# Performance work log

Measured on AMD Instinct MI355X. Metric: run time of the kernel, lower is better.

The kernel has to match this reference:

```python
import jax, jax.numpy as jnp
import numpy as np

FG_THR = 0.7
BG_THR = 0.3
NUM_PER_IMAGE = 256
NUM_POS_MAX = int(NUM_PER_IMAGE * 0.5)  # positive_ratio = 0.5
BBOX_W = (1.0, 1.0, 1.0, 1.0)
BETA = 1.0 / 9.0


def _permute(t, C):
    # N x (A*C) x H x W -> N x (H*W*A) x C, matching RPNLoss.permute
    N, _, H, W = t.shape
    t = t.reshape(N, -1, C, H, W)
    t = jnp.transpose(t, (0, 3, 4, 1, 2))
    return t.reshape(N, -1, C)


def _iou(a, b):
    # a: [N,4], b: [M,4] -> [N,M] (with +1 box convention, as in source)
    x_tl = jnp.maximum(a[:, None, 0], b[None, :, 0])
    y_tl = jnp.maximum(a[:, None, 1], b[None, :, 1])
    x_rb = jnp.minimum(a[:, None, 2], b[None, :, 2])
    y_rb = jnp.minimum(a[:, None, 3], b[None, :, 3])
    inter = jnp.clip(x_rb - x_tl + 1.0, 0.0) * jnp.clip(y_rb - y_tl + 1.0, 0.0)
    area1 = (a[:, 2] - a[:, 0] + 1.0) * (a[:, 3] - a[:, 1] + 1.0)
    area2 = (b[:, 2] - b[:, 0] + 1.0) * (b[:, 3] - b[:, 1] + 1.0)
    return inter / (area1[:, None] + area2[None, :] - inter)


def _encode(anchors, targets):
    ws = anchors[:, 2] - anchors[:, 0] + 1.0
    hs = anchors[:, 3] - anchors[:, 1] + 1.0
    x_ctr = anchors[:, 0] + 0.5 * ws
    y_ctr = anchors[:, 1] + 0.5 * hs
    t_ws = targets[:, 2] - targets[:, 0] + 1.0
    t_hs = targets[:, 3] - targets[:, 1] + 1.0
    t_x = targets[:, 0] + 0.5 * t_ws
    t_y = targets[:, 1] + 0.5 * t_hs
    wx, wy, ww, wh = BBOX_W
    tx = wx * (t_x - x_ctr) / ws
    ty = wy * (t_y - y_ctr) / hs
    tw = ww * jnp.log(t_ws / ws)
    th = wh * jnp.log(t_hs / hs)
    return jnp.stack([tx, ty, tw, th], axis=1)


def _bce_logits(l, t):
    return jnp.maximum(l, 0.0) - l * t + jnp.log1p(jnp.exp(-jnp.abs(l)))


def _per_image(anchor, logit, breg, size, target, key):
    N = anchor.shape[0]
    ious = _iou(anchor, target)  # [N, M]
    vals = ious.max(axis=1)
    ori = jnp.argmax(ious, axis=1).astype(jnp.int32)
    inds = jnp.where(vals < BG_THR, -1, ori)
    inds = jnp.where((vals >= BG_THR) & (vals < FG_THR), -2, inds)
    # low-quality matches: anchors achieving the per-target max IoU keep their argmax
    col_max = ious.max(axis=0)
    restore = (ious == col_max[None, :]).any(axis=1)
    inds = jnp.where(restore, ori, inds)
    # filter_anchors: keep anchors fully inside the image (size = (h, w))
    inside = (anchor[:, 0] >= 0) & (anchor[:, 1] >= 0) & \
             (anchor[:, 2] <= size[1] - 1.0) & (anchor[:, 3] <= size[0] - 1.0)
    inds = jnp.where(inside, inds, -2)

    pos = inds >= 0
    neg = inds == -1
    # random sampling via random priorities + fixed-size top_k with validity masks
    r = jax.random.uniform(key, (N,))
    pos_vals, pos_idx = jax.lax.top_k(jnp.where(pos, r, -1.0), NUM_POS_MAX)
    valid_pos = pos_vals >= 0.0
    num_pos = valid_pos.sum()
    neg_vals, neg_idx = jax.lax.top_k(jnp.where(neg, r, -1.0), NUM_PER_IMAGE)
    valid_neg = (neg_vals >= 0.0) & (jnp.arange(NUM_PER_IMAGE) < (NUM_PER_IMAGE - num_pos))

    # classification loss terms (BCE with logits); pos target 1, neg target 0
    vp = valid_pos.astype(logit.dtype)
    vn = valid_neg.astype(logit.dtype)
    cls_sum = jnp.sum(_bce_logits(logit[pos_idx], 1.0) * vp) + \
              jnp.sum(_bce_logits(logit[neg_idx], 0.0) * vn)
    count = num_pos + valid_neg.sum()

    m = jnp.clip(inds[pos_idx], 0, None)
    offsets = _encode(anchor[pos_idx], target[m])
    diff = jnp.abs(breg[pos_idx] - offsets)
    sl1 = jnp.where(diff < BETA, 0.5 * diff * diff / BETA, diff - 0.5 * BETA)
    reg_sum = jnp.sum(sl1 * vp[:, None])
    return cls_sum, count, reg_sum


def reference(anchors, logits, bbox_regs, sizes, targets):
    B = anchors.shape[0]
    log = _permute(logits, 1)[..., 0]      # [B, H*W*A]
    breg = _permute(bbox_regs, 4)          # [B, H*W*A, 4]
    keys = jax.random.split(jax.random.key(42), B)
    cls_s, cnt, reg_s = jax.vmap(_per_image)(anchors, log, breg, sizes, targets, keys)
    total = jnp.sum(cnt).astype(anchors.dtype)
    cls_loss = jnp.sum(cls_s) / total
    reg_loss = jnp.sum(reg_s) / total
    return jnp.stack([cls_loss, reg_loss])


def setup_inputs() -> dict:
    key = jax.random.key(0)
    ks = jax.random.split(key, 10)
    B, A, H, W, M = 4, 3, 168, 256, 32
    N = H * W * A
    IMG_H, IMG_W = 800.0, 1333.0
    x1 = jax.random.uniform(ks[0], (B, N)) * 1200.0
    y1 = jax.random.uniform(ks[1], (B, N)) * 700.0
    aw = jax.random.uniform(ks[2], (B, N)) * 300.0 + 16.0
    ah = jax.random.uniform(ks[3], (B, N)) * 300.0 + 16.0
    anchors = jnp.stack([x1, y1, x1 + aw, y1 + ah], axis=-1)  # some out of image -> filtered
    tx1 = jax.random.uniform(ks[4], (B, M)) * 1000.0
    ty1 = jax.random.uniform(ks[5], (B, M)) * 500.0
    tw = jax.random.uniform(ks[6], (B, M)) * 250.0 + 30.0
    th = jax.random.uniform(ks[7], (B, M)) * 200.0 + 30.0
    targets = jnp.stack([tx1, ty1, jnp.minimum(tx1 + tw, IMG_W - 1.0),
                         jnp.minimum(ty1 + th, IMG_H - 1.0)], axis=-1)
    logits = jax.random.normal(ks[8], (B, A, H, W), dtype=jnp.float32)
    bbox_regs = jax.random.normal(ks[9], (B, 4 * A, H, W), dtype=jnp.float32) * 0.1
    sizes = jnp.tile(jnp.array([IMG_H, IMG_W], dtype=jnp.float32), (B, 1))
    return {"anchors": anchors, "logits": logits, "bbox_regs": bbox_regs,
            "sizes": sizes, "targets": targets}
```

## Files before the change

kernel.cpp:

```cpp
#include <hip/hip_runtime.h>
#include <stdint.h>

#define Bn 4
#define An 3
#define Hn 168
#define Wn 256
#define Mn 32
#define HWn (Hn*Wn)
#define Nn (HWn*An)
#define POS_CAP 8192
#define BND_CAP 2048
#define NPERIM 256
#define NPOSMAX 128
#define FG_THR 0.7f
#define BG_THR 0.3f
#define BETA (1.0f/9.0f)

#define NBLK 126
#define APT 4
#define STRIDE (NBLK * 256)
#define SEG 1024

#define OFF_POSCNT 0
#define OFF_BNDCNT 4
#define OFF_BOUND  8
#define OFF_NEED   12
#define OFF_COUNT  16
#define OFF_CLS    17
#define OFF_REG    18
#define OFF_DONE   19
#define OFF_KEYS   24
#define OFF_PCM    32
#define OFF_NSEGC  16160
#define OFF_PHIST  16664
#define OFF_PLIST  532760
#define OFF_BLIST  598296
#define OFF_NLIST  614680

__device__ __forceinline__ uint32_t rotl32(uint32_t v, int n) { return (v << n) | (v >> (32 - n)); }

__device__ __forceinline__ void tf2x32(uint32_t k0, uint32_t k1, uint32_t x0, uint32_t x1,
                                       uint32_t& o0, uint32_t& o1) {
    uint32_t k2 = k0 ^ k1 ^ 0x1BD11BDAu;
    x0 += k0; x1 += k1;
    x0 += x1; x1 = rotl32(x1, 13); x1 ^= x0;
    x0 += x1; x1 = rotl32(x1, 15); x1 ^= x0;
    x0 += x1; x1 = rotl32(x1, 26); x1 ^= x0;
    x0 += x1; x1 = rotl32(x1, 6);  x1 ^= x0;
    x0 += k1; x1 += k2 + 1u;
    x0 += x1; x1 = rotl32(x1, 17); x1 ^= x0;
    x0 += x1; x1 = rotl32(x1, 29); x1 ^= x0;
    x0 += x1; x1 = rotl32(x1, 16); x1 ^= x0;
    x0 += x1; x1 = rotl32(x1, 24); x1 ^= x0;
    x0 += k2; x1 += k0 + 2u;
    x0 += x1; x1 = rotl32(x1, 13); x1 ^= x0;
    x0 += x1; x1 = rotl32(x1, 15); x1 ^= x0;
    x0 += x1; x1 = rotl32(x1, 26); x1 ^= x0;
    x0 += x1; x1 = rotl32(x1, 6);  x1 ^= x0;
    x0 += k0; x1 += k1 + 3u;
    x0 += x1; x1 = rotl32(x1, 17); x1 ^= x0;
    x0 += x1; x1 = rotl32(x1, 29); x1 ^= x0;
    x0 += x1; x1 = rotl32(x1, 16); x1 ^= x0;
    x0 += x1; x1 = rotl32(x1, 24); x1 ^= x0;
    x0 += k1; x1 += k2 + 4u;
    x0 += x1; x1 = rotl32(x1, 13); x1 ^= x0;
    x0 += x1; x1 = rotl32(x1, 15); x1 ^= x0;
    x0 += x1; x1 = rotl32(x1, 26); x1 ^= x0;
    x0 += x1; x1 = rotl32(x1, 6);  x1 ^= x0;
    x0 += k2; x1 += k0 + 5u;
    o0 = x0; o1 = x1;
}

__device__ __forceinline__ uint32_t rng_m23(uint32_t k0, uint32_t k1, uint32_t i) {
    uint32_t o0, o1;
    tf2x32(k0, k1, 0u, i, o0, o1);
    return (o0 ^ o1) >> 9;
}

__device__ __forceinline__ float iou_one(float a0, float a1, float a2, float a3,
                                         float t0, float t1, float t2, float t3) {
    float xtl = fmaxf(a0, t0), ytl = fmaxf(a1, t1);
    float xrb = fminf(a2, t2), yrb = fminf(a3, t3);
    float iw = fmaxf(xrb - xtl + 1.0f, 0.0f);
    float ih = fmaxf(yrb - ytl + 1.0f, 0.0f);
    float inter = iw * ih;
    float area1 = (a2 - a0 + 1.0f) * (a3 - a1 + 1.0f);
    float area2 = (t2 - t0 + 1.0f) * (t3 - t1 + 1.0f);
    return inter * __builtin_amdgcn_rcpf(area1 + area2 - inter);
}

__global__ void __launch_bounds__(256) k1_colmax(const float* __restrict__ anchors,
                                                 const float* __restrict__ targets,
                                                 uint32_t* __restrict__ ws) {
    int b = blockIdx.y, j = blockIdx.x, tid = threadIdx.x;
    if (b == 0 && j == 0) {
        if (tid < 24) ws[tid] = 0u;
        if (tid == 0) {
            for (int bb = 0; bb < Bn; ++bb) {
                uint32_t o0, o1;
                tf2x32(0u, 42u, 0u, (uint32_t)bb, o0, o1);
                ws[OFF_KEYS + 2*bb] = o0; ws[OFF_KEYS + 2*bb + 1] = o1;
            }
        }
    }
    __shared__ float part[4][Mn];
    int base = j * 256 + tid;
    float4 a[APT];
    #pragma unroll
    for (int k = 0; k < APT; ++k)
        a[k] = ((const float4*)anchors)[b * Nn + base + k * STRIDE];
    float cm[Mn];
    #pragma unroll 4
    for (int t = 0; t < Mn; ++t) {
        float4 tv = ((const float4*)targets)[b * Mn + t];
        float m0 = 0.0f;
        #pragma unroll
        for (int k = 0; k < APT; ++k)
            m0 = fmaxf(m0, iou_one(a[k].x, a[k].y, a[k].z, a[k].w, tv.x, tv.y, tv.z, tv.w));
        cm[t] = m0;
    }
    #pragma unroll
    for (int t = 0; t < Mn; ++t) {
        #pragma unroll
        for (int o = 32; o > 0; o >>= 1) cm[t] = fmaxf(cm[t], __shfl_xor(cm[t], o, 64));
    }
    int wid = tid >> 6, lane = tid & 63;
    if (lane == 0) {
        #pragma unroll
        for (int t = 0; t < Mn; ++t) part[wid][t] = cm[t];
    }
    __syncthreads();
    if (tid < Mn) {
        float v = fmaxf(fmaxf(part[0][tid], part[1][tid]),
                        fmaxf(part[2][tid], part[3][tid]));
        ws[OFF_PCM + ((size_t)b * NBLK + j) * Mn + tid] = __float_as_uint(v);
    }
}

__global__ void __launch_bounds__(256) k2_cat(const float* __restrict__ anchors,
                                              const float* __restrict__ targets,
                                              const float* __restrict__ sizes,
                                              uint32_t* __restrict__ ws) {
    int b = blockIdx.y, j = blockIdx.x, tid = threadIdx.x;
    __shared__ float cmf[Mn];
    __shared__ float redf[256];
    __shared__ uint32_t lh[1024];
    __shared__ uint32_t segcnt;
    {
        int t = tid & 31, sub = tid >> 5;
        float acc = 0.0f;
        for (int jj = sub; jj < NBLK; jj += 8)
            acc = fmaxf(acc, __uint_as_float(ws[OFF_PCM + ((size_t)b * NBLK + jj) * Mn + t]));
        redf[tid] = acc;
        __syncthreads();
        if (sub == 0) {
            #pragma unroll
            for (int q = 1; q < 8; ++q) acc = fmaxf(acc, redf[t + 32 * q]);
            cmf[t] = acc;
        }
    }
    #pragma unroll
    for (int q = 0; q < 4; ++q) lh[tid + 256 * q] = 0u;
    if (tid == 0) segcnt = 0u;
    __syncthreads();

    int base = j * 256 + tid;
    float4 av[APT];
    #pragma unroll
    for (int k = 0; k < APT; ++k)
        av[k] = ((const float4*)anchors)[b * Nn + base + k * STRIDE];
    float rowmax[APT]; int ori[APT]; bool restore[APT];
    #pragma unroll
    for (int k = 0; k < APT; ++k) { rowmax[k] = -1.0f; ori[k] = 0; restore[k] = false; }
    #pragma unroll 4
    for (int t = 0; t < Mn; ++t) {
        float4 tv = ((const float4*)targets)[b * Mn + t];
        float cmv = cmf[t];
        #pragma unroll
        for (int k = 0; k < APT; ++k) {
            float iou = iou_one(av[k].x, av[k].y, av[k].z, av[k].w, tv.x, tv.y, tv.z, tv.w);
            if (iou > rowmax[k]) { rowmax[k] = iou; ori[k] = t; }
            restore[k] = restore[k] || (iou == cmv);
        }
    }
    float sh = sizes[b * 2 + 0], sw = sizes[b * 2 + 1];
    uint32_t key0 = ws[OFF_KEYS + 2 * b], key1 = ws[OFF_KEYS + 2 * b + 1];
    int lane = tid & 63;
    unsigned long long lt_mask = (lane == 63) ? 0x7FFFFFFFFFFFFFFFull : ((1ull << lane) - 1ull);
    uint2* nseg = (uint2*)(ws + OFF_NLIST) + (size_t)(b * NBLK + j) * SEG;
    #pragma unroll
    for (int k = 0; k < APT; ++k) {
        int i = base + k * STRIDE;
        bool inside = (av[k].x >= 0.0f) && (av[k].y >= 0.0f) &&
                      (av[k].z <= sw - 1.0f) && (av[k].w <= sh - 1.0f);
        uint32_t cat = 0;
        if (inside) {
            if (restore[k] || rowmax[k] >= FG_THR) cat = 2;
            else if (rowmax[k] < BG_THR) cat = 1;
        }
        uint32_t m = rng_m23(key0, key1, (uint32_t)i);
        unsigned long long pmask = __ballot(cat == 2u);
        if (pmask) {
            int leader = __ffsll((long long)pmask) - 1;
            uint32_t bb = 0;
            if (lane == leader) bb = atomicAdd(&ws[OFF_POSCNT + b], (uint32_t)__popcll(pmask));
            bb = __shfl(bb, leader, 64);
            if (cat == 2u) {
                uint32_t p = bb + (uint32_t)__popcll(pmask & lt_mask);
                if (p < POS_CAP)
                    ((uint2*)(ws + OFF_PLIST))[(size_t)b * POS_CAP + p] =
                        make_uint2(m, (uint32_t)i | ((uint32_t)ori[k] << 17));
            }
        }
        unsigned long long nmask = __ballot(cat == 1u);
        if (nmask) {
            int leader = __ffsll((long long)nmask) - 1;
            uint32_t bb = 0;
            if (lane == leader) bb = atomicAdd(&segcnt, (uint32_t)__popcll(nmask));
            bb = __shfl(bb, leader, 64);
            if (cat == 1u) {
                uint32_t p = bb + (uint32_t)__popcll(nmask & lt_mask);
                nseg[p] = make_uint2(m, (uint32_t)i);
                atomicAdd(&lh[m >> 13], 1u);
            }
        }
    }
    __syncthreads();
    uint32_t* slice = ws + OFF_PHIST + ((size_t)b * NBLK + j) * 1024;
    #pragma unroll
    for (int q = 0; q < 4; ++q) slice[tid + 256 * q] = lh[tid + 256 * q];
    if (tid == 0) ws[OFF_NSEGC + b * NBLK + j] = segcnt;
}

__global__ void __launch_bounds__(256) k25_bound(uint32_t* __restrict__ ws) {
    int b = blockIdx.x, t = threadIdx.x;
    __shared__ uint32_t csum[256];
    uint4 h = make_uint4(0, 0, 0, 0);
    const uint32_t* ph = ws + OFF_PHIST + (size_t)b * NBLK * 1024;
    for (int s = 0; s < NBLK; ++s) {
        uint4 v = ((const uint4*)(ph + (size_t)s * 1024))[t];
        h.x += v.x; h.y += v.y; h.z += v.z; h.w += v.w;
    }
    uint32_t sum = h.x + h.y + h.z + h.w;
    csum[t] = sum;
    __syncthreads();
    for (int off = 1; off < 256; off <<= 1) {
        uint32_t mine = csum[t];
        uint32_t add = (t + off < 256) ? csum[t + off] : 0u;
        __syncthreads();
        csum[t] = mine + add;
        __syncthreads();
    }
    uint32_t pc = ws[OFF_POSCNT + b];
    int num_pos = (pc < (uint32_t)NPOSMAX) ? (int)pc : NPOSMAX;
    int k_neg = NPERIM - num_pos;
    uint32_t total = csum[0];
    if ((int)total < k_neg) {
        if (t == 0) {
            ws[OFF_BOUND + b] = 0xFFFFFFFFu;
            ws[OFF_NEED + b] = 0u;
            atomicAdd(&ws[OFF_COUNT], (uint32_t)(num_pos + (int)total));
        }
        return;
    }
    uint32_t incl = csum[t];
    uint32_t next = (t < 255) ? csum[t + 1] : 0u;
    if ((int)incl >= k_neg && (int)next < k_neg) {
        int cum = (int)next;
        uint32_t hv[4] = { h.x, h.y, h.z, h.w };
        int boundary = -1, needed = 0;
        #pragma unroll
        for (int q = 3; q >= 0; --q) {
            int c = (int)hv[q];
            if (cum + c >= k_neg) { boundary = 4 * t + q; needed = k_neg - cum; break; }
            cum += c;
        }
        ws[OFF_BOUND + b] = (uint32_t)boundary;
        ws[OFF_NEED + b] = (uint32_t)needed;
        atomicAdd(&ws[OFF_COUNT], (uint32_t)(num_pos + k_neg));
    }
}

__global__ void __launch_bounds__(256) k3_neg(const float* __restrict__ logits,
                                              uint32_t* __restrict__ ws) {
    int b = blockIdx.y, j = blockIdx.x;
    int bd = (int)(int32_t)ws[OFF_BOUND + b];
    int cnt = (int)ws[OFF_NSEGC + b * NBLK + j];
    const uint2* nseg = (const uint2*)(ws + OFF_NLIST) + (size_t)(b * NBLK + j) * SEG;
    float local = 0.0f;
    for (int idx = (int)threadIdx.x; idx < cnt; idx += 256) {
        uint2 e = nseg[idx];
        int bk = (int)(e.x >> 13);
        if (bk > bd) {
            int i = (int)e.y;
            int a = i % An, hw = i / An;
            float l = logits[(b * An + a) * HWn + hw];
            local += fmaxf(l, 0.0f) + log1pf(expf(-fabsf(l)));
        } else if (bk == bd) {
            uint32_t q = atomicAdd(&ws[OFF_BNDCNT + b], 1u);
            if (q < BND_CAP)
                ((uint2*)(ws + OFF_BLIST))[(size_t)b * BND_CAP + q] = e;
        }
    }
    __shared__ float red[256];
    red[threadIdx.x] = local;
    __syncthreads();
    for (int s = 128; s > 0; s >>= 1) {
        if ((int)threadIdx.x < s) red[threadIdx.x] += red[threadIdx.x + s];
        __syncthreads();
    }
    if (threadIdx.x == 0 && red[0] != 0.0f) atomicAdd((float*)&ws[OFF_CLS], red[0]);
}

__device__ __forceinline__ bool sel_less(uint2 a, uint2 b) {
    return (a.x > b.x) || (a.x == b.x && a.y < b.y);
}

__device__ void bitonic_sort_shared(uint2* buf, int n) {
    for (int k = 2; k <= n; k <<= 1) {
        for (int j = k >> 1; j > 0; j >>= 1) {
            for (int t = (int)threadIdx.x; t < n; t += 256) {
                int ixj = t ^ j;
                if (ixj > t) {
                    uint2 x = buf[t], y = buf[ixj];
                    bool up = ((t & k) == 0);
                    bool sw = up ? sel_less(y, x) : sel_less(x, y);
                    if (sw) { buf[t] = y; buf[ixj] = x; }
                }
            }
            __syncthreads();
        }
    }
}

__global__ void __launch_bounds__(256) k4_final(const float* __restrict__ anchors,
                                                const float* __restrict__ targets,
                                                const float* __restrict__ logits,
                                                const float* __restrict__ bregs,
                                                uint32_t* __restrict__ ws,
                                                float* __restrict__ out) {
    int b = blockIdx.x, tid = threadIdx.x;
    __shared__ uint2 buf[BND_CAP];
    __shared__ float red[256];
    float cls = 0.0f, reg = 0.0f;

    uint32_t pcu = ws[OFF_POSCNT + b];
    int pc = (pcu < (uint32_t)POS_CAP) ? (int)pcu : POS_CAP;
    const uint2* plist = (const uint2*)(ws + OFF_PLIST) + (size_t)b * POS_CAP;
    int psel = (pc < NPOSMAX) ? pc : NPOSMAX;
    bool use_buf = false;
    if (pc > NPOSMAX) {
        int n = (pc < BND_CAP) ? pc : BND_CAP;
        for (int t = tid; t < n; t += 256) buf[t] = plist[t];
        int npad = 1; while (npad < n) npad <<= 1;
        for (int t = tid; t < npad; t += 256) if (t >= n) buf[t] = make_uint2(0u, 0xFFFFFFFFu);
        __syncthreads();
        bitonic_sort_shared(buf, npad);
        use_buf = true;
        psel = (NPOSMAX < n) ? NPOSMAX : n;
    }
    for (int t = tid; t < psel; t += 256) {
        uint32_t packed = use_buf ? buf[t].y : plist[t].y;
        int i = (int)(packed & 0x1FFFFu);
        int ori = (int)(packed >> 17);
        int a = i % An, hw = i / An;
        float l = logits[(b * An + a) * HWn + hw];
        cls += fmaxf(l, 0.0f) - l + log1pf(expf(-fabsf(l)));
        float4 av = ((const float4*)anchors)[b * Nn + i];
        float4 tv = ((const float4*)targets)[b * Mn + ori];
        float aws = av.z - av.x + 1.0f, ahs = av.w - av.y + 1.0f;
        float axc = av.x + 0.5f * aws, ayc = av.y + 0.5f * ahs;
        float tws = tv.z - tv.x + 1.0f, ths = tv.w - tv.y + 1.0f;
        float txc = tv.x + 0.5f * tws, tyc = tv.y + 0.5f * ths;
        float off0 = (txc - axc) / aws;
        float off1 = (tyc - ayc) / ahs;
        float off2 = logf(tws / aws);
        float off3 = logf(ths / ahs);
        float br0 = bregs[(b * 12 + a * 4 + 0) * HWn + hw];
        float br1 = bregs[(b * 12 + a * 4 + 1) * HWn + hw];
        float br2 = bregs[(b * 12 + a * 4 + 2) * HWn + hw];
        float br3 = bregs[(b * 12 + a * 4 + 3) * HWn + hw];
        float d;
        d = fabsf(br0 - off0); reg += (d < BETA) ? 0.5f * d * d / BETA : d - 0.5f * BETA;
        d = fabsf(br1 - off1); reg += (d < BETA) ? 0.5f * d * d / BETA : d - 0.5f * BETA;
        d = fabsf(br2 - off2); reg += (d < BETA) ? 0.5f * d * d / BETA : d - 0.5f * BETA;
        d = fabsf(br3 - off3); reg += (d < BETA) ? 0.5f * d * d / BETA : d - 0.5f * BETA;
    }
    __syncthreads();

    int need = (int)ws[OFF_NEED + b];
    if (need > 0) {
        uint32_t nbu = ws[OFF_BNDCNT + b];
        int nb = (nbu < (uint32_t)BND_CAP) ? (int)nbu : BND_CAP;
        const uint2* blist = (const uint2*)(ws + OFF_BLIST) + (size_t)b * BND_CAP;
        for (int t = tid; t < nb; t += 256) buf[t] = blist[t];
        int npad = 1; while (npad < nb) npad <<= 1;
        for (int t = tid; t < npad; t += 256) if (t >= nb) buf[t] = make_uint2(0u, 0xFFFFFFFFu);
        __syncthreads();
        bitonic_sort_shared(buf, npad);
        int sel = (need < nb) ? need : nb;
        for (int t = tid; t < sel; t += 256) {
            int i = (int)buf[t].y;
            int a = i % An, hw = i / An;
            float l = logits[(b * An + a) * HWn + hw];
            cls += fmaxf(l, 0.0f) + log1pf(expf(-fabsf(l)));
        }
    }

    red[tid] = cls;
    __syncthreads();
    for (int s = 128; s > 0; s >>= 1) {
        if (tid < s) red[tid] += red[tid + s];
        __syncthreads();
    }
    if (tid == 0 && red[0] != 0.0f) atomicAdd((float*)&ws[OFF_CLS], red[0]);
    __syncthreads();
    red[tid] = reg;
    __syncthreads();
    for (int s = 128; s > 0; s >>= 1) {
        if (tid < s) red[tid] += red[tid + s];
        __syncthreads();
    }
    if (tid == 0) {
        if (red[0] != 0.0f) atomicAdd((float*)&ws[OFF_REG], red[0]);
        __threadfence();
        uint32_t old = atomicAdd(&ws[OFF_DONE], 1u);
        if (old == Bn - 1) {
            float cls_tot = __uint_as_float(atomicAdd(&ws[OFF_CLS], 0u));
            float reg_tot = __uint_as_float(atomicAdd(&ws[OFF_REG], 0u));
            float cnt = (float)atomicAdd(&ws[OFF_COUNT], 0u);
            out[0] = cls_tot / cnt;
            out[1] = reg_tot / cnt;
        }
    }
}

extern "C" void kernel_launch(void* const* d_in, const int* in_sizes, int n_in,
                              void* d_out, int out_size, void* d_ws, size_t ws_size,
                              hipStream_t stream) {
    const float* anchors = (const float*)d_in[0];
    const float* logits  = (const float*)d_in[1];
    const float* bregs   = (const float*)d_in[2];
    const float* sizes   = (const float*)d_in[3];
    const float* targets = (const float*)d_in[4];
    float* out = (float*)d_out;
    uint32_t* ws = (uint32_t*)d_ws;

    k1_colmax<<<dim3(NBLK, Bn), dim3(256), 0, stream>>>(anchors, targets, ws);
    k2_cat<<<dim3(NBLK, Bn), dim3(256), 0, stream>>>(anchors, targets, sizes, ws);
    k25_bound<<<dim3(Bn), dim3(256), 0, stream>>>(ws);
    k3_neg<<<dim3(NBLK, Bn), dim3(256), 0, stream>>>(logits, ws);
    k4_final<<<dim3(Bn), dim3(256), 0, stream>>>(anchors, targets, logits, bregs, ws, out);
}
```

Baseline: 158.1 us.

## Fuse all RPN loss stages into one cooperative kernel with grid syncs

```diff
diff --git a/kernel.cpp b/kernel.cpp
--- a/kernel.cpp
+++ b/kernel.cpp
@@ -1,5 +1,8 @@
 #include <hip/hip_runtime.h>
+#include <hip/hip_cooperative_groups.h>
 #include <stdint.h>
+
+namespace cg = cooperative_groups;
 
 #define Bn 4
 #define An 3
@@ -32,10 +35,11 @@
 #define OFF_KEYS   24
 #define OFF_PCM    32
 #define OFF_NSEGC  16160
-#define OFF_PHIST  16664
-#define OFF_PLIST  532760
-#define OFF_BLIST  598296
-#define OFF_NLIST  614680
+#define OFF_PLIST  16664
+#define OFF_BLIST  82200
+#define OFF_NLIST  98584
+#define OFF_WPCM   1130776
+#define OFF_GHIST  1195288
 
 __device__ __forceinline__ uint32_t rotl32(uint32_t v, int n) { return (v << n) | (v >> (32 - n)); }
 
@@ -89,229 +93,6 @@
     return inter * __builtin_amdgcn_rcpf(area1 + area2 - inter);
 }
 
-__global__ void __launch_bounds__(256) k1_colmax(const float* __restrict__ anchors,
-                                                 const float* __restrict__ targets,
-                                                 uint32_t* __restrict__ ws) {
-    int b = blockIdx.y, j = blockIdx.x, tid = threadIdx.x;
-    if (b == 0 && j == 0) {
-        if (tid < 24) ws[tid] = 0u;
-        if (tid == 0) {
-            for (int bb = 0; bb < Bn; ++bb) {
-                uint32_t o0, o1;
-                tf2x32(0u, 42u, 0u, (uint32_t)bb, o0, o1);
-                ws[OFF_KEYS + 2*bb] = o0; ws[OFF_KEYS + 2*bb + 1] = o1;
-            }
-        }
-    }
-    __shared__ float part[4][Mn];
-    int base = j * 256 + tid;
-    float4 a[APT];
-    #pragma unroll
-    for (int k = 0; k < APT; ++k)
-        a[k] = ((const float4*)anchors)[b * Nn + base + k * STRIDE];
-    float cm[Mn];
-    #pragma unroll 4
-    for (int t = 0; t < Mn; ++t) {
-        float4 tv = ((const float4*)targets)[b * Mn + t];
-        float m0 = 0.0f;
-        #pragma unroll
-        for (int k = 0; k < APT; ++k)
-            m0 = fmaxf(m0, iou_one(a[k].x, a[k].y, a[k].z, a[k].w, tv.x, tv.y, tv.z, tv.w));
-        cm[t] = m0;
-    }
-    #pragma unroll
-    for (int t = 0; t < Mn; ++t) {
-        #pragma unroll
-        for (int o = 32; o > 0; o >>= 1) cm[t] = fmaxf(cm[t], __shfl_xor(cm[t], o, 64));
-    }
-    int wid = tid >> 6, lane = tid & 63;
-    if (lane == 0) {
-        #pragma unroll
-        for (int t = 0; t < Mn; ++t) part[wid][t] = cm[t];
-    }
-    __syncthreads();
-    if (tid < Mn) {
-        float v = fmaxf(fmaxf(part[0][tid], part[1][tid]),
-                        fmaxf(part[2][tid], part[3][tid]));
-        ws[OFF_PCM + ((size_t)b * NBLK + j) * Mn + tid] = __float_as_uint(v);
-    }
-}
-
-__global__ void __launch_bounds__(256) k2_cat(const float* __restrict__ anchors,
-                                              const float* __restrict__ targets,
-                                              const float* __restrict__ sizes,
-                                              uint32_t* __restrict__ ws) {
-    int b = blockIdx.y, j = blockIdx.x, tid = threadIdx.x;
-    __shared__ float cmf[Mn];
-    __shared__ float redf[256];
-    __shared__ uint32_t lh[1024];
-    __shared__ uint32_t segcnt;
-    {
-        int t = tid & 31, sub = tid >> 5;
-        float acc = 0.0f;
-        for (int jj = sub; jj < NBLK; jj += 8)
-            acc = fmaxf(acc, __uint_as_float(ws[OFF_PCM + ((size_t)b * NBLK + jj) * Mn + t]));
-        redf[tid] = acc;
-        __syncthreads();
-        if (sub == 0) {
-            #pragma unroll
-            for (int q = 1; q < 8; ++q) acc = fmaxf(acc, redf[t + 32 * q]);
-            cmf[t] = acc;
-        }
-    }
-    #pragma unroll
-    for (int q = 0; q < 4; ++q) lh[tid + 256 * q] = 0u;
-    if (tid == 0) segcnt = 0u;
-    __syncthreads();
-
-    int base = j * 256 + tid;
-    float4 av[APT];
-    #pragma unroll
-    for (int k = 0; k < APT; ++k)
-        av[k] = ((const float4*)anchors)[b * Nn + base + k * STRIDE];
-    float rowmax[APT]; int ori[APT]; bool restore[APT];
-    #pragma unroll
-    for (int k = 0; k < APT; ++k) { rowmax[k] = -1.0f; ori[k] = 0; restore[k] = false; }
-    #pragma unroll 4
-    for (int t = 0; t < Mn; ++t) {
-        float4 tv = ((const float4*)targets)[b * Mn + t];
-        float cmv = cmf[t];
-        #pragma unroll
-        for (int k = 0; k < APT; ++k) {
-            float iou = iou_one(av[k].x, av[k].y, av[k].z, av[k].w, tv.x, tv.y, tv.z, tv.w);
-            if (iou > rowmax[k]) { rowmax[k] = iou; ori[k] = t; }
-            restore[k] = restore[k] || (iou == cmv);
-        }
-    }
-    float sh = sizes[b * 2 + 0], sw = sizes[b * 2 + 1];
-    uint32_t key0 = ws[OFF_KEYS + 2 * b], key1 = ws[OFF_KEYS + 2 * b + 1];
-    int lane = tid & 63;
-    unsigned long long lt_mask = (lane == 63) ? 0x7FFFFFFFFFFFFFFFull : ((1ull << lane) - 1ull);
-    uint2* nseg = (uint2*)(ws + OFF_NLIST) + (size_t)(b * NBLK + j) * SEG;
-    #pragma unroll
-    for (int k = 0; k < APT; ++k) {
-        int i = base + k * STRIDE;
-        bool inside = (av[k].x >= 0.0f) && (av[k].y >= 0.0f) &&
-                      (av[k].z <= sw - 1.0f) && (av[k].w <= sh - 1.0f);
-        uint32_t cat = 0;
-        if (inside) {
-            if (restore[k] || rowmax[k] >= FG_THR) cat = 2;
-            else if (rowmax[k] < BG_THR) cat = 1;
-        }
-        uint32_t m = rng_m23(key0, key1, (uint32_t)i);
-        unsigned long long pmask = __ballot(cat == 2u);
-        if (pmask) {
-            int leader = __ffsll((long long)pmask) - 1;
-            uint32_t bb = 0;
-            if (lane == leader) bb = atomicAdd(&ws[OFF_POSCNT + b], (uint32_t)__popcll(pmask));
-            bb = __shfl(bb, leader, 64);
-            if (cat == 2u) {
-                uint32_t p = bb + (uint32_t)__popcll(pmask & lt_mask);
-                if (p < POS_CAP)
-                    ((uint2*)(ws + OFF_PLIST))[(size_t)b * POS_CAP + p] =
-                        make_uint2(m, (uint32_t)i | ((uint32_t)ori[k] << 17));
-            }
-        }
-        unsigned long long nmask = __ballot(cat == 1u);
-        if (nmask) {
-            int leader = __ffsll((long long)nmask) - 1;
-            uint32_t bb = 0;
-            if (lane == leader) bb = atomicAdd(&segcnt, (uint32_t)__popcll(nmask));
-            bb = __shfl(bb, leader, 64);
-            if (cat == 1u) {
-                uint32_t p = bb + (uint32_t)__popcll(nmask & lt_mask);
-                nseg[p] = make_uint2(m, (uint32_t)i);
-                atomicAdd(&lh[m >> 13], 1u);
-            }
-        }
-    }
-    __syncthreads();
-    uint32_t* slice = ws + OFF_PHIST + ((size_t)b * NBLK + j) * 1024;
-    #pragma unroll
-    for (int q = 0; q < 4; ++q) slice[tid + 256 * q] = lh[tid + 256 * q];
-    if (tid == 0) ws[OFF_NSEGC + b * NBLK + j] = segcnt;
-}
-
-__global__ void __launch_bounds__(256) k25_bound(uint32_t* __restrict__ ws) {
-    int b = blockIdx.x, t = threadIdx.x;
-    __shared__ uint32_t csum[256];
-    uint4 h = make_uint4(0, 0, 0, 0);
-    const uint32_t* ph = ws + OFF_PHIST + (size_t)b * NBLK * 1024;
-    for (int s = 0; s < NBLK; ++s) {
-        uint4 v = ((const uint4*)(ph + (size_t)s * 1024))[t];
-        h.x += v.x; h.y += v.y; h.z += v.z; h.w += v.w;
-    }
-    uint32_t sum = h.x + h.y + h.z + h.w;
-    csum[t] = sum;
-    __syncthreads();
-    for (int off = 1; off < 256; off <<= 1) {
-        uint32_t mine = csum[t];
-        uint32_t add = (t + off < 256) ? csum[t + off] : 0u;
-        __syncthreads();
-        csum[t] = mine + add;
-        __syncthreads();
-    }
-    uint32_t pc = ws[OFF_POSCNT + b];
-    int num_pos = (pc < (uint32_t)NPOSMAX) ? (int)pc : NPOSMAX;
-    int k_neg = NPERIM - num_pos;
-    uint32_t total = csum[0];
-    if ((int)total < k_neg) {
-        if (t == 0) {
-            ws[OFF_BOUND + b] = 0xFFFFFFFFu;
-            ws[OFF_NEED + b] = 0u;
-            atomicAdd(&ws[OFF_COUNT], (uint32_t)(num_pos + (int)total));
-        }
-        return;
-    }
-    uint32_t incl = csum[t];
-    uint32_t next = (t < 255) ? csum[t + 1] : 0u;
-    if ((int)incl >= k_neg && (int)next < k_neg) {
-        int cum = (int)next;
-        uint32_t hv[4] = { h.x, h.y, h.z, h.w };
-        int boundary = -1, needed = 0;
-        #pragma unroll
-        for (int q = 3; q >= 0; --q) {
-            int c = (int)hv[q];
-            if (cum + c >= k_neg) { boundary = 4 * t + q; needed = k_neg - cum; break; }
-            cum += c;
-        }
-        ws[OFF_BOUND + b] = (uint32_t)boundary;
-        ws[OFF_NEED + b] = (uint32_t)needed;
-        atomicAdd(&ws[OFF_COUNT], (uint32_t)(num_pos + k_neg));
-    }
-}
-
-__global__ void __launch_bounds__(256) k3_neg(const float* __restrict__ logits,
-                                              uint32_t* __restrict__ ws) {
-    int b = blockIdx.y, j = blockIdx.x;
-    int bd = (int)(int32_t)ws[OFF_BOUND + b];
-    int cnt = (int)ws[OFF_NSEGC + b * NBLK + j];
-    const uint2* nseg = (const uint2*)(ws + OFF_NLIST) + (size_t)(b * NBLK + j) * SEG;
-    float local = 0.0f;
-    for (int idx = (int)threadIdx.x; idx < cnt; idx += 256) {
-        uint2 e = nseg[idx];
-        int bk = (int)(e.x >> 13);
-        if (bk > bd) {
-            int i = (int)e.y;
-            int a = i % An, hw = i / An;
-            float l = logits[(b * An + a) * HWn + hw];
-            local += fmaxf(l, 0.0f) + log1pf(expf(-fabsf(l)));
-        } else if (bk == bd) {
-            uint32_t q = atomicAdd(&ws[OFF_BNDCNT + b], 1u);
-            if (q < BND_CAP)
-                ((uint2*)(ws + OFF_BLIST))[(size_t)b * BND_CAP + q] = e;
-        }
-    }
-    __shared__ float red[256];
-    red[threadIdx.x] = local;
-    __syncthreads();
-    for (int s = 128; s > 0; s >>= 1) {
-        if ((int)threadIdx.x < s) red[threadIdx.x] += red[threadIdx.x + s];
-        __syncthreads();
-    }
-    if (threadIdx.x == 0 && red[0] != 0.0f) atomicAdd((float*)&ws[OFF_CLS], red[0]);
-}
-
 __device__ __forceinline__ bool sel_less(uint2 a, uint2 b) {
     return (a.x > b.x) || (a.x == b.x && a.y < b.y);
 }
@@ -333,104 +114,328 @@
     }
 }
 
-__global__ void __launch_bounds__(256) k4_final(const float* __restrict__ anchors,
-                                                const float* __restrict__ targets,
-                                                const float* __restrict__ logits,
-                                                const float* __restrict__ bregs,
-                                                uint32_t* __restrict__ ws,
-                                                float* __restrict__ out) {
-    int b = blockIdx.x, tid = threadIdx.x;
-    __shared__ uint2 buf[BND_CAP];
-    __shared__ float red[256];
-    float cls = 0.0f, reg = 0.0f;
-
-    uint32_t pcu = ws[OFF_POSCNT + b];
-    int pc = (pcu < (uint32_t)POS_CAP) ? (int)pcu : POS_CAP;
-    const uint2* plist = (const uint2*)(ws + OFF_PLIST) + (size_t)b * POS_CAP;
-    int psel = (pc < NPOSMAX) ? pc : NPOSMAX;
-    bool use_buf = false;
-    if (pc > NPOSMAX) {
-        int n = (pc < BND_CAP) ? pc : BND_CAP;
-        for (int t = tid; t < n; t += 256) buf[t] = plist[t];
-        int npad = 1; while (npad < n) npad <<= 1;
-        for (int t = tid; t < npad; t += 256) if (t >= n) buf[t] = make_uint2(0u, 0xFFFFFFFFu);
-        __syncthreads();
-        bitonic_sort_shared(buf, npad);
-        use_buf = true;
-        psel = (NPOSMAX < n) ? NPOSMAX : n;
-    }
-    for (int t = tid; t < psel; t += 256) {
-        uint32_t packed = use_buf ? buf[t].y : plist[t].y;
-        int i = (int)(packed & 0x1FFFFu);
-        int ori = (int)(packed >> 17);
-        int a = i % An, hw = i / An;
-        float l = logits[(b * An + a) * HWn + hw];
-        cls += fmaxf(l, 0.0f) - l + log1pf(expf(-fabsf(l)));
-        float4 av = ((const float4*)anchors)[b * Nn + i];
-        float4 tv = ((const float4*)targets)[b * Mn + ori];
-        float aws = av.z - av.x + 1.0f, ahs = av.w - av.y + 1.0f;
-        float axc = av.x + 0.5f * aws, ayc = av.y + 0.5f * ahs;
-        float tws = tv.z - tv.x + 1.0f, ths = tv.w - tv.y + 1.0f;
-        float txc = tv.x + 0.5f * tws, tyc = tv.y + 0.5f * ths;
-        float off0 = (txc - axc) / aws;
-        float off1 = (tyc - ayc) / ahs;
-        float off2 = logf(tws / aws);
-        float off3 = logf(ths / ahs);
-        float br0 = bregs[(b * 12 + a * 4 + 0) * HWn + hw];
-        float br1 = bregs[(b * 12 + a * 4 + 1) * HWn + hw];
-        float br2 = bregs[(b * 12 + a * 4 + 2) * HWn + hw];
-        float br3 = bregs[(b * 12 + a * 4 + 3) * HWn + hw];
-        float d;
-        d = fabsf(br0 - off0); reg += (d < BETA) ? 0.5f * d * d / BETA : d - 0.5f * BETA;
-        d = fabsf(br1 - off1); reg += (d < BETA) ? 0.5f * d * d / BETA : d - 0.5f * BETA;
-        d = fabsf(br2 - off2); reg += (d < BETA) ? 0.5f * d * d / BETA : d - 0.5f * BETA;
-        d = fabsf(br3 - off3); reg += (d < BETA) ? 0.5f * d * d / BETA : d - 0.5f * BETA;
+struct ShP1 { float part[4][Mn]; };
+struct ShP2 { float cmf[Mn]; float redf[256]; uint32_t lh[1024]; uint32_t segcnt; };
+struct ShP3 { uint32_t csum[256]; };
+struct ShP45 { uint2 buf[BND_CAP]; float red[256]; };
+union ShU { ShP1 p1; ShP2 p2; ShP3 p3; ShP45 p45; };
+
+__global__ void __launch_bounds__(256, 2)
+fused(const float* __restrict__ anchors, const float* __restrict__ targets,
+      const float* __restrict__ sizes, const float* __restrict__ logits,
+      const float* __restrict__ bregs, uint32_t* __restrict__ ws,
+      float* __restrict__ out)
+{
+    cg::grid_group grid = cg::this_grid();
+    __shared__ ShU smem;
+    const int j = blockIdx.x, b = blockIdx.y, tid = threadIdx.x;
+    const int wid = tid >> 6, lane = tid & 63;
+
+    if (j == 0 && b == 0) {
+        if (tid < 24) ws[tid] = 0u;
+        for (int q = tid; q < Bn * 1024; q += 256) ws[OFF_GHIST + q] = 0u;
+        if (tid == 0) {
+            for (int bb = 0; bb < Bn; ++bb) {
+                uint32_t o0, o1;
+                tf2x32(0u, 42u, 0u, (uint32_t)bb, o0, o1);
+                ws[OFF_KEYS + 2*bb] = o0; ws[OFF_KEYS + 2*bb + 1] = o1;
+            }
+        }
+    }
+
+    const int base = j * 256 + tid;
+    float4 av[APT];
+    #pragma unroll
+    for (int k = 0; k < APT; ++k)
+        av[k] = ((const float4*)anchors)[b * Nn + base + k * STRIDE];
+
+    float rowmax[APT]; int ori[APT]; uint32_t tie[APT];
+    #pragma unroll
+    for (int k = 0; k < APT; ++k) { rowmax[k] = -1.0f; ori[k] = 0; tie[k] = 0u; }
+
+    uint32_t* wp = ws + OFF_WPCM + ((((size_t)b * NBLK + j) * 4 + wid) << 5);
+
+    #pragma unroll 4
+    for (int t = 0; t < Mn; ++t) {
+        float4 tv = ((const float4*)targets)[b * Mn + t];
+        float io[APT];
+        float m0 = 0.0f;
+        #pragma unroll
+        for (int k = 0; k < APT; ++k) {
+            io[k] = iou_one(av[k].x, av[k].y, av[k].z, av[k].w, tv.x, tv.y, tv.z, tv.w);
+            if (io[k] > rowmax[k]) { rowmax[k] = io[k]; ori[k] = t; }
+            m0 = fmaxf(m0, io[k]);
+        }
+        #pragma unroll
+        for (int o = 32; o > 0; o >>= 1) m0 = fmaxf(m0, __shfl_xor(m0, o, 64));
+        if (lane == 0) {
+            smem.p1.part[wid][t] = m0;
+            wp[t] = __float_as_uint(m0);
+        }
+        #pragma unroll
+        for (int k = 0; k < APT; ++k)
+            tie[k] |= (io[k] == m0) ? (1u << t) : 0u;
     }
     __syncthreads();
-
-    int need = (int)ws[OFF_NEED + b];
-    if (need > 0) {
-        uint32_t nbu = ws[OFF_BNDCNT + b];
-        int nb = (nbu < (uint32_t)BND_CAP) ? (int)nbu : BND_CAP;
-        const uint2* blist = (const uint2*)(ws + OFF_BLIST) + (size_t)b * BND_CAP;
-        for (int t = tid; t < nb; t += 256) buf[t] = blist[t];
-        int npad = 1; while (npad < nb) npad <<= 1;
-        for (int t = tid; t < npad; t += 256) if (t >= nb) buf[t] = make_uint2(0u, 0xFFFFFFFFu);
-        __syncthreads();
-        bitonic_sort_shared(buf, npad);
-        int sel = (need < nb) ? need : nb;
-        for (int t = tid; t < sel; t += 256) {
-            int i = (int)buf[t].y;
+    if (tid < Mn) {
+        float v = fmaxf(fmaxf(smem.p1.part[0][tid], smem.p1.part[1][tid]),
+                        fmaxf(smem.p1.part[2][tid], smem.p1.part[3][tid]));
+        ws[OFF_PCM + ((size_t)b * NBLK + j) * Mn + tid] = __float_as_uint(v);
+    }
+
+    grid.sync();
+
+    {
+        int t = tid & 31, sub = tid >> 5;
+        float acc = 0.0f;
+        for (int jj = sub; jj < NBLK; jj += 8)
+            acc = fmaxf(acc, __uint_as_float(ws[OFF_PCM + ((size_t)b * NBLK + jj) * Mn + t]));
+        smem.p2.redf[tid] = acc;
+        __syncthreads();
+        if (sub == 0) {
+            #pragma unroll
+            for (int q = 1; q < 8; ++q) acc = fmaxf(acc, smem.p2.redf[t + 32 * q]);
+            smem.p2.cmf[t] = acc;
+        }
+    }
+    #pragma unroll
+    for (int q = 0; q < 4; ++q) smem.p2.lh[tid + 256 * q] = 0u;
+    if (tid == 0) smem.p2.segcnt = 0u;
+    __syncthreads();
+
+    uint32_t eqmask;
+    {
+        bool eq = (lane < Mn) ? (__uint_as_float(wp[lane]) == smem.p2.cmf[lane]) : false;
+        eqmask = (uint32_t)__ballot(eq);
+    }
+
+    {
+        const float szh = sizes[b * 2 + 0], szw = sizes[b * 2 + 1];
+        const uint32_t key0 = ws[OFF_KEYS + 2 * b], key1 = ws[OFF_KEYS + 2 * b + 1];
+        unsigned long long lt_mask = (lane == 63) ? 0x7FFFFFFFFFFFFFFFull
+                                                  : ((1ull << lane) - 1ull);
+        uint2* nseg = (uint2*)(ws + OFF_NLIST) + (size_t)(b * NBLK + j) * SEG;
+        #pragma unroll
+        for (int k = 0; k < APT; ++k) {
+            int i = base + k * STRIDE;
+            bool inside = (av[k].x >= 0.0f) && (av[k].y >= 0.0f) &&
+                          (av[k].z <= szw - 1.0f) && (av[k].w <= szh - 1.0f);
+            bool restore = (tie[k] & eqmask) != 0u;
+            uint32_t cat = 0;
+            if (inside) {
+                if (restore || rowmax[k] >= FG_THR) cat = 2;
+                else if (rowmax[k] < BG_THR) cat = 1;
+            }
+            uint32_t m = rng_m23(key0, key1, (uint32_t)i);
+            unsigned long long pmask = __ballot(cat == 2u);
+            if (pmask) {
+                int leader = __ffsll((long long)pmask) - 1;
+                uint32_t bb = 0;
+                if (lane == leader) bb = atomicAdd(&ws[OFF_POSCNT + b], (uint32_t)__popcll(pmask));
+                bb = __shfl(bb, leader, 64);
+                if (cat == 2u) {
+                    uint32_t p = bb + (uint32_t)__popcll(pmask & lt_mask);
+                    if (p < POS_CAP)
+                        ((uint2*)(ws + OFF_PLIST))[(size_t)b * POS_CAP + p] =
+                            make_uint2(m, (uint32_t)i | ((uint32_t)ori[k] << 17));
+                }
+            }
+            unsigned long long nmask = __ballot(cat == 1u);
+            if (nmask) {
+                int leader = __ffsll((long long)nmask) - 1;
+                uint32_t bb = 0;
+                if (lane == leader) bb = atomicAdd(&smem.p2.segcnt, (uint32_t)__popcll(nmask));
+                bb = __shfl(bb, leader, 64);
+                if (cat == 1u) {
+                    uint32_t p = bb + (uint32_t)__popcll(nmask & lt_mask);
+                    nseg[p] = make_uint2(m, (uint32_t)i);
+                    atomicAdd(&smem.p2.lh[m >> 13], 1u);
+                }
+            }
+        }
+    }
+    __syncthreads();
+    {
+        uint32_t* gh = ws + OFF_GHIST + b * 1024;
+        #pragma unroll
+        for (int q = 0; q < 4; ++q) {
+            uint32_t v = smem.p2.lh[tid + 256 * q];
+            if (v) atomicAdd(&gh[tid + 256 * q], v);
+        }
+        if (tid == 0) ws[OFF_NSEGC + b * NBLK + j] = smem.p2.segcnt;
+    }
+
+    grid.sync();
+
+    if (j == 0) {
+        uint4 h = ((const uint4*)(ws + OFF_GHIST + (size_t)b * 1024))[tid];
+        uint32_t sum = h.x + h.y + h.z + h.w;
+        smem.p3.csum[tid] = sum;
+        __syncthreads();
+        for (int off = 1; off < 256; off <<= 1) {
+            uint32_t mine = smem.p3.csum[tid];
+            uint32_t add = (tid + off < 256) ? smem.p3.csum[tid + off] : 0u;
+            __syncthreads();
+            smem.p3.csum[tid] = mine + add;
+            __syncthreads();
+        }
+        uint32_t pc = ws[OFF_POSCNT + b];
+        int num_pos = (pc < (uint32_t)NPOSMAX) ? (int)pc : NPOSMAX;
+        int k_neg = NPERIM - num_pos;
+        uint32_t total = smem.p3.csum[0];
+        if ((int)total < k_neg) {
+            if (tid == 0) {
+                ws[OFF_BOUND + b] = 0xFFFFFFFFu;
+                ws[OFF_NEED + b] = 0u;
+                atomicAdd(&ws[OFF_COUNT], (uint32_t)(num_pos + (int)total));
+            }
+        } else {
+            uint32_t incl = smem.p3.csum[tid];
+            uint32_t next = (tid < 255) ? smem.p3.csum[tid + 1] : 0u;
+            if ((int)incl >= k_neg && (int)next < k_neg) {
+                int cum = (int)next;
+                uint32_t hv[4] = { h.x, h.y, h.z, h.w };
+                int boundary = -1, needed = 0;
+                #pragma unroll
+                for (int q = 3; q >= 0; --q) {
+                    int c = (int)hv[q];
+                    if (cum + c >= k_neg) { boundary = 4 * tid + q; needed = k_neg - cum; break; }
+                    cum += c;
+                }
+                ws[OFF_BOUND + b] = (uint32_t)boundary;
+                ws[OFF_NEED + b] = (uint32_t)needed;
+                atomicAdd(&ws[OFF_COUNT], (uint32_t)(num_pos + k_neg));
+            }
+        }
+    }
+
+    grid.sync();
+
+    {
+        int bd = (int)(int32_t)ws[OFF_BOUND + b];
+        int cnt = (int)ws[OFF_NSEGC + b * NBLK + j];
+        const uint2* nsegr = (const uint2*)(ws + OFF_NLIST) + (size_t)(b * NBLK + j) * SEG;
+        float local = 0.0f;
+        for (int idx = tid; idx < cnt; idx += 256) {
+            uint2 e = nsegr[idx];
+            int bk = (int)(e.x >> 13);
+            if (bk > bd) {
+                int i = (int)e.y;
+                int a = i % An, hw = i / An;
+                float l = logits[(b * An + a) * HWn + hw];
+                local += fmaxf(l, 0.0f) + log1pf(expf(-fabsf(l)));
+            } else if (bk == bd) {
+                uint32_t q = atomicAdd(&ws[OFF_BNDCNT + b], 1u);
+                if (q < BND_CAP)
+                    ((uint2*)(ws + OFF_BLIST))[(size_t)b * BND_CAP + q] = e;
+            }
+        }
+        smem.p45.red[tid] = local;
+        __syncthreads();
+        for (int s = 128; s > 0; s >>= 1) {
+            if (tid < s) smem.p45.red[tid] += smem.p45.red[tid + s];
+            __syncthreads();
+        }
+        if (tid == 0 && smem.p45.red[0] != 0.0f)
+            atomicAdd((float*)&ws[OFF_CLS], smem.p45.red[0]);
+    }
+
+    grid.sync();
+
+    if (j != 0) return;
+    {
+        uint2* buf = smem.p45.buf;
+        float* red = smem.p45.red;
+        float cls = 0.0f, reg = 0.0f;
+
+        uint32_t pcu = ws[OFF_POSCNT + b];
+        int pc = (pcu < (uint32_t)POS_CAP) ? (int)pcu : POS_CAP;
+        const uint2* plist = (const uint2*)(ws + OFF_PLIST) + (size_t)b * POS_CAP;
+        int psel = (pc < NPOSMAX) ? pc : NPOSMAX;
+        bool use_buf = false;
+        if (pc > NPOSMAX) {
+            int n = (pc < BND_CAP) ? pc : BND_CAP;
+            for (int t = tid; t < n; t += 256) buf[t] = plist[t];
+            int npad = 1; while (npad < n) npad <<= 1;
+            for (int t = tid; t < npad; t += 256) if (t >= n) buf[t] = make_uint2(0u, 0xFFFFFFFFu);
+            __syncthreads();
+            bitonic_sort_shared(buf, npad);
+            use_buf = true;
+            psel = (NPOSMAX < n) ? NPOSMAX : n;
+        }
+        for (int t = tid; t < psel; t += 256) {
+            uint32_t packed = use_buf ? buf[t].y : plist[t].y;
+            int i = (int)(packed & 0x1FFFFu);
+            int orit = (int)(packed >> 17);
             int a = i % An, hw = i / An;
             float l = logits[(b * An + a) * HWn + hw];
-            cls += fmaxf(l, 0.0f) + log1pf(expf(-fabsf(l)));
-        }
-    }
-
-    red[tid] = cls;
-    __syncthreads();
-    for (int s = 128; s > 0; s >>= 1) {
-        if (tid < s) red[tid] += red[tid + s];
-        __syncthreads();
-    }
-    if (tid == 0 && red[0] != 0.0f) atomicAdd((float*)&ws[OFF_CLS], red[0]);
-    __syncthreads();
-    red[tid] = reg;
-    __syncthreads();
-    for (int s = 128; s > 0; s >>= 1) {
-        if (tid < s) red[tid] += red[tid + s];
-        __syncthreads();
-    }
-    if (tid == 0) {
-        if (red[0] != 0.0f) atomicAdd((float*)&ws[OFF_REG], red[0]);
-        __threadfence();
-        uint32_t old = atomicAdd(&ws[OFF_DONE], 1u);
-        if (old == Bn - 1) {
-            float cls_tot = __uint_as_float(atomicAdd(&ws[OFF_CLS], 0u));
-            float reg_tot = __uint_as_float(atomicAdd(&ws[OFF_REG], 0u));
-            float cnt = (float)atomicAdd(&ws[OFF_COUNT], 0u);
-            out[0] = cls_tot / cnt;
-            out[1] = reg_tot / cnt;
+            cls += fmaxf(l, 0.0f) - l + log1pf(expf(-fabsf(l)));
+            float4 avx = ((const float4*)anchors)[b * Nn + i];
+            float4 tv = ((const float4*)targets)[b * Mn + orit];
+            float aws = avx.z - avx.x + 1.0f, ahs = avx.w - avx.y + 1.0f;
+            float axc = avx.x + 0.5f * aws, ayc = avx.y + 0.5f * ahs;
+            float tws = tv.z - tv.x + 1.0f, ths = tv.w - tv.y + 1.0f;
+            float txc = tv.x + 0.5f * tws, tyc = tv.y + 0.5f * ths;
+            float off0 = (txc - axc) / aws;
+            float off1 = (tyc - ayc) / ahs;
+            float off2 = logf(tws / aws);
+            float off3 = logf(ths / ahs);
+            float br0 = bregs[(b * 12 + a * 4 + 0) * HWn + hw];
+            float br1 = bregs[(b * 12 + a * 4 + 1) * HWn + hw];
+            float br2 = bregs[(b * 12 + a * 4 + 2) * HWn + hw];
+            float br3 = bregs[(b * 12 + a * 4 + 3) * HWn + hw];
+            float d;
+            d = fabsf(br0 - off0); reg += (d < BETA) ? 0.5f * d * d / BETA : d - 0.5f * BETA;
+            d = fabsf(br1 - off1); reg += (d < BETA) ? 0.5f * d * d / BETA : d - 0.5f * BETA;
+            d = fabsf(br2 - off2); reg += (d < BETA) ? 0.5f * d * d / BETA : d - 0.5f * BETA;
+            d = fabsf(br3 - off3); reg += (d < BETA) ? 0.5f * d * d / BETA : d - 0.5f * BETA;
+        }
+        __syncthreads();
+
+        int need = (int)ws[OFF_NEED + b];
+        if (need > 0) {
+            uint32_t nbu = ws[OFF_BNDCNT + b];
+            int nb = (nbu < (uint32_t)BND_CAP) ? (int)nbu : BND_CAP;
+            const uint2* blist = (const uint2*)(ws + OFF_BLIST) + (size_t)b * BND_CAP;
+            for (int t = tid; t < nb; t += 256) buf[t] = blist[t];
+            int npad = 1; while (npad < nb) npad <<= 1;
+            for (int t = tid; t < npad; t += 256) if (t >= nb) buf[t] = make_uint2(0u, 0xFFFFFFFFu);
+            __syncthreads();
+            bitonic_sort_shared(buf, npad);
+            int sel = (need < nb) ? need : nb;
+            for (int t = tid; t < sel; t += 256) {
+                int i = (int)buf[t].y;
+                int a = i % An, hw = i / An;
+                float l = logits[(b * An + a) * HWn + hw];
+                cls += fmaxf(l, 0.0f) + log1pf(expf(-fabsf(l)));
+            }
+        }
+
+        red[tid] = cls;
+        __syncthreads();
+        for (int s = 128; s > 0; s >>= 1) {
+            if (tid < s) red[tid] += red[tid + s];
+            __syncthreads();
+        }
+        if (tid == 0 && red[0] != 0.0f) atomicAdd((float*)&ws[OFF_CLS], red[0]);
+        __syncthreads();
+        red[tid] = reg;
+        __syncthreads();
+        for (int s = 128; s > 0; s >>= 1) {
+            if (tid < s) red[tid] += red[tid + s];
+            __syncthreads();
+        }
+        if (tid == 0) {
+            if (red[0] != 0.0f) atomicAdd((float*)&ws[OFF_REG], red[0]);
+            __threadfence();
+            uint32_t old = atomicAdd(&ws[OFF_DONE], 1u);
+            if (old == Bn - 1) {
+                float cls_tot = __uint_as_float(atomicAdd(&ws[OFF_CLS], 0u));
+                float reg_tot = __uint_as_float(atomicAdd(&ws[OFF_REG], 0u));
+                float cnt = (float)atomicAdd(&ws[OFF_COUNT], 0u);
+                out[0] = cls_tot / cnt;
+                out[1] = reg_tot / cnt;
+            }
         }
     }
 }
@@ -446,9 +451,8 @@
     float* out = (float*)d_out;
     uint32_t* ws = (uint32_t*)d_ws;
 
-    k1_colmax<<<dim3(NBLK, Bn), dim3(256), 0, stream>>>(anchors, targets, ws);
-    k2_cat<<<dim3(NBLK, Bn), dim3(256), 0, stream>>>(anchors, targets, sizes, ws);
-    k25_bound<<<dim3(Bn), dim3(256), 0, stream>>>(ws);
-    k3_neg<<<dim3(NBLK, Bn), dim3(256), 0, stream>>>(logits, ws);
-    k4_final<<<dim3(Bn), dim3(256), 0, stream>>>(anchors, targets, logits, bregs, ws, out);
-}
+    void* args[] = { (void*)&anchors, (void*)&targets, (void*)&sizes,
+                     (void*)&logits, (void*)&bregs, (void*)&ws, (void*)&out };
+    hipLaunchCooperativeKernel((const void*)fused, dim3(NBLK, Bn), dim3(256),
+                               args, 0, stream);
+}
```

Result: slower. 356.3 us (+125.3%).
